# Kernel tuning notes

Measured on AMD Instinct MI355X. Metric: run time of the kernel, lower is better.

## Reference

```python
import jax, jax.numpy as jnp
import numpy as np

KH, KW = 3, 3
H_OUT, W_OUT = 62, 62

def setup_inputs() -> dict:
    key = jax.random.key(0)
    k1, k2 = jax.random.split(key)
    x = jax.random.normal(k1, (16, 32, 64, 64), dtype=jnp.float32)
    weight = jax.random.normal(k2, (H_OUT, W_OUT, 64, 32, KH, KW), dtype=jnp.float32) * 0.01
    return {"x": x, "weight": weight}

def reference(x, weight):
    # Unfold: patches[b,c,kh,kw,i,j] = x[b,c,i+kh,j+kw]; small fixed 3x3 loop is fine.
    patches = jnp.stack([
        jnp.stack([x[:, :, kh:kh + H_OUT, kw:kw + W_OUT] for kw in range(KW)], axis=2)
        for kh in range(KH)
    ], axis=2)  # [B, C_in, kH, kW, H_out, W_out]
    # Per-position (no weight sharing) contraction over c_in, kh, kw.
    out = jnp.einsum('bcklij,ijockl->boij', patches, weight)
    return jax.nn.sigmoid(out)
```

## Files before the change

### kernel.cpp

```cpp
#include <hip/hip_runtime.h>

#define HO 62
#define WO 62
#define CIN 32
#define COUT 64
#define BATCH 16
#define KROW 288
#define JT 4
#define COLS 6

typedef float f4a4 __attribute__((ext_vector_type(4), aligned(4)));

__global__ __launch_bounds__(256, 4)
void lc2d_kernel(const float* __restrict__ x,
                 const float* __restrict__ wgt,
                 float* __restrict__ out) {
    __shared__ __align__(16) float win[CIN][3][COLS][BATCH];

    const int blk = blockIdx.x;
    const int i  = blk % HO;
    const int j0 = (blk / HO) * JT;

    const int t = threadIdx.x;

    for (int r = t; r < BATCH * CIN * 3; r += 256) {
        const int b   = r & 15;
        const int ckh = r >> 4;
        const int c   = ckh / 3;
        const int kh  = ckh % 3;
        const float* src = x + (((b * CIN + c) * 64) + (i + kh)) * 64;
        #pragma unroll
        for (int cc = 0; cc < COLS; cc++) {
            int col = j0 + cc;
            if (col > 63) col = 63;
            win[c][kh][cc][b] = src[col];
        }
    }
    __syncthreads();

    const int wsel = t >> 6;
    const int o    = t & 63;

    const float* wj[JT];
    #pragma unroll
    for (int jj = 0; jj < JT; jj++) {
        int pj = i * WO + (j0 + jj);
        if (pj > HO * WO - 1) pj = HO * WO - 1;
        wj[jj] = wgt + (size_t)pj * (COUT * KROW) + o * KROW;
    }

    float acc[JT][4];
    #pragma unroll
    for (int jj = 0; jj < JT; jj++)
        #pragma unroll
        for (int bb = 0; bb < 4; bb++) acc[jj][bb] = 0.0f;

    const float* xbase = &win[0][0][0][wsel * 4];

    for (int c = 0; c < CIN; c++) {
        float wq[JT][9];
        #pragma unroll
        for (int jj = 0; jj < JT; jj++) {
            const float* p = wj[jj] + c * 9;
            const f4a4 wA = *(const f4a4*)p;
            const f4a4 wB = *(const f4a4*)(p + 4);
            wq[jj][0] = wA.x; wq[jj][1] = wA.y; wq[jj][2] = wA.z; wq[jj][3] = wA.w;
            wq[jj][4] = wB.x; wq[jj][5] = wB.y; wq[jj][6] = wB.z; wq[jj][7] = wB.w;
            wq[jj][8] = p[8];
        }
        #pragma unroll
        for (int kh = 0; kh < 3; kh++) {
            float4 xv[COLS];
            const float* xb = xbase + (c * 3 + kh) * (COLS * BATCH);
            #pragma unroll
            for (int cc = 0; cc < COLS; cc++)
                xv[cc] = *(const float4*)(xb + cc * BATCH);
            #pragma unroll
            for (int jj = 0; jj < JT; jj++) {
                #pragma unroll
                for (int kw = 0; kw < 3; kw++) {
                    const float w = wq[jj][kh * 3 + kw];
                    const float4 xx = xv[jj + kw];
                    acc[jj][0] += w * xx.x;
                    acc[jj][1] += w * xx.y;
                    acc[jj][2] += w * xx.z;
                    acc[jj][3] += w * xx.w;
                }
            }
        }
    }

    #pragma unroll
    for (int bb = 0; bb < 4; bb++) {
        const int b = wsel * 4 + bb;
        float* op = out + (((size_t)(b * COUT + o) * HO + i) * WO + j0);
        float2 s0;
        s0.x = 1.0f / (1.0f + __expf(-acc[0][bb]));
        s0.y = 1.0f / (1.0f + __expf(-acc[1][bb]));
        *(float2*)op = s0;
        if (j0 + 3 < WO) {
            float2 s1;
            s1.x = 1.0f / (1.0f + __expf(-acc[2][bb]));
            s1.y = 1.0f / (1.0f + __expf(-acc[3][bb]));
            *((float2*)op + 1) = s1;
        }
    }
}

extern "C" void kernel_launch(void* const* d_in, const int* in_sizes, int n_in,
                              void* d_out, int out_size, void* d_ws, size_t ws_size,
                              hipStream_t stream) {
    const float* x   = (const float*)d_in[0];
    const float* wgt = (const float*)d_in[1];
    float* out       = (float*)d_out;
    const int grid = HO * ((WO + JT - 1) / JT);
    lc2d_kernel<<<dim3(grid), dim3(256), 0, stream>>>(x, wgt, out);
}
```

Measured before the change: 571.7 us.

## Stream weights into LDS with async global_load_lds double buffering and XCD remap

Weights are now staged into a swizzled, double-buffered LDS tile with direct global-to-LDS loads, prefetching the next two-channel phase while the current one is computed. The x input window is no longer staged in shared memory and is read directly from global memory per batch. The tile width drops from four to two output columns, and block indices are remapped so neighbouring tiles share an XCD. The goal is coalesced, overlapped weight streaming from HBM, at the cost of more blocks, more per-phase barriers, and redundant x reads from global memory or cache.

```diff
diff --git a/kernel.cpp b/kernel.cpp
--- a/kernel.cpp
+++ b/kernel.cpp
@@ -1,4 +1,5 @@
 #include <hip/hip_runtime.h>
+#include <stdint.h>
 
 #define HO 62
 #define WO 62
@@ -6,48 +7,64 @@
 #define COUT 64
 #define BATCH 16
 #define KROW 288
-#define JT 4
-#define COLS 6
+#define JT 2
+#define NJT (WO / JT)
+#define ROWS 128
+#define PC 2
+#define NPH (CIN / PC)
+#define PH_DW (PC * 9)
+#define RSTRIDE 32
+#define SLOTS (ROWS * RSTRIDE)
+#define NXCD 8
 
-typedef float f4a4 __attribute__((ext_vector_type(4), aligned(4)));
+typedef const __attribute__((address_space(1))) void* gptr_t;
+typedef __attribute__((address_space(3))) void* lptr_t;
 
 __global__ __launch_bounds__(256, 4)
 void lc2d_kernel(const float* __restrict__ x,
                  const float* __restrict__ wgt,
                  float* __restrict__ out) {
-    __shared__ __align__(16) float win[CIN][3][COLS][BATCH];
+    __shared__ __align__(16) float wlds[2][SLOTS];
 
-    const int blk = blockIdx.x;
-    const int i  = blk % HO;
-    const int j0 = (blk / HO) * JT;
+    const int orig = blockIdx.x;
+    const int nwg  = HO * NJT;
+    const int qch  = nwg / NXCD, rch = nwg % NXCD;
+    const int xcd  = orig % NXCD, pos = orig / NXCD;
+    const int wg   = ((xcd < rch) ? xcd * (qch + 1)
+                                  : rch * (qch + 1) + (xcd - rch) * qch) + pos;
+    const int i  = wg / NJT;
+    const int j0 = (wg % NJT) * JT;
 
-    const int t = threadIdx.x;
-
-    for (int r = t; r < BATCH * CIN * 3; r += 256) {
-        const int b   = r & 15;
-        const int ckh = r >> 4;
-        const int c   = ckh / 3;
-        const int kh  = ckh % 3;
-        const float* src = x + (((b * CIN + c) * 64) + (i + kh)) * 64;
-        #pragma unroll
-        for (int cc = 0; cc < COLS; cc++) {
-            int col = j0 + cc;
-            if (col > 63) col = 63;
-            win[c][kh][cc][b] = src[col];
-        }
-    }
-    __syncthreads();
-
+    const int t    = threadIdx.x;
     const int wsel = t >> 6;
     const int o    = t & 63;
+    const int ws_u = __builtin_amdgcn_readfirstlane(wsel);
 
-    const float* wj[JT];
+    const float* wbase = wgt + (size_t)(i * WO + j0) * (COUT * KROW);
+
+    int goff[16];
     #pragma unroll
-    for (int jj = 0; jj < JT; jj++) {
-        int pj = i * WO + (j0 + jj);
-        if (pj > HO * WO - 1) pj = HO * WO - 1;
-        wj[jj] = wgt + (size_t)pj * (COUT * KROW) + o * KROW;
+    for (int g = 0; g < 16; g++) {
+        const int s   = wsel * 1024 + g * 64 + o;
+        const int row = s >> 5;
+        const int k   = s & 31;
+        const int l   = k ^ ((row & 7) << 2);
+        int src;
+        if (l < 24) {
+            const int cc = l / 12;
+            int r2 = l % 12; if (r2 > 8) r2 = 8;
+            src = row * KROW + cc * 9 + r2;
+        } else {
+            src = row * KROW;
+        }
+        goff[g] = src;
     }
+
+    #pragma unroll
+    for (int g = 0; g < 16; g++)
+        __builtin_amdgcn_global_load_lds((gptr_t)(wbase + goff[g]),
+                                         (lptr_t)&wlds[0][ws_u * 1024 + g * 64],
+                                         4, 0, 0);
 
     float acc[JT][4];
     #pragma unroll
@@ -55,55 +72,81 @@
         #pragma unroll
         for (int bb = 0; bb < 4; bb++) acc[jj][bb] = 0.0f;
 
-    const float* xbase = &win[0][0][0][wsel * 4];
+    const float* xp[4];
+    #pragma unroll
+    for (int bb = 0; bb < 4; bb++)
+        xp[bb] = x + ((size_t)(wsel * 4 + bb) * CIN) * 4096 + i * 64 + j0;
 
-    for (int c = 0; c < CIN; c++) {
-        float wq[JT][9];
+    const int swz = (o & 7) << 2;
+
+    __syncthreads();
+
+    int cur = 0;
+    for (int p = 0; p < NPH; p++) {
+        if (p + 1 < NPH) {
+            const float* wsrc = wbase + (p + 1) * PH_DW;
+            #pragma unroll
+            for (int g = 0; g < 16; g++)
+                __builtin_amdgcn_global_load_lds((gptr_t)(wsrc + goff[g]),
+                                                 (lptr_t)&wlds[cur ^ 1][ws_u * 1024 + g * 64],
+                                                 4, 0, 0);
+        }
+
         #pragma unroll
-        for (int jj = 0; jj < JT; jj++) {
-            const float* p = wj[jj] + c * 9;
-            const f4a4 wA = *(const f4a4*)p;
-            const f4a4 wB = *(const f4a4*)(p + 4);
-            wq[jj][0] = wA.x; wq[jj][1] = wA.y; wq[jj][2] = wA.z; wq[jj][3] = wA.w;
-            wq[jj][4] = wB.x; wq[jj][5] = wB.y; wq[jj][6] = wB.z; wq[jj][7] = wB.w;
-            wq[jj][8] = p[8];
-        }
-        #pragma unroll
-        for (int kh = 0; kh < 3; kh++) {
-            float4 xv[COLS];
-            const float* xb = xbase + (c * 3 + kh) * (COLS * BATCH);
-            #pragma unroll
-            for (int cc = 0; cc < COLS; cc++)
-                xv[cc] = *(const float4*)(xb + cc * BATCH);
+        for (int cc = 0; cc < PC; cc++) {
+            const int c = p * PC + cc;
+
+            float4 wA[JT], wB[JT]; float w8[JT];
             #pragma unroll
             for (int jj = 0; jj < JT; jj++) {
+                const int base = (jj * 64 + o) * RSTRIDE + cc * 12;
+                wA[jj] = *(const float4*)&wlds[cur][(base + 0) ^ swz];
+                wB[jj] = *(const float4*)&wlds[cur][(base + 4) ^ swz];
+                w8[jj] = wlds[cur][(base + 8) ^ swz];
+            }
+
+            #pragma unroll
+            for (int kh = 0; kh < 3; kh++) {
+                float2 xa[4], xb[4];
                 #pragma unroll
-                for (int kw = 0; kw < 3; kw++) {
-                    const float w = wq[jj][kh * 3 + kw];
-                    const float4 xx = xv[jj + kw];
-                    acc[jj][0] += w * xx.x;
-                    acc[jj][1] += w * xx.y;
-                    acc[jj][2] += w * xx.z;
-                    acc[jj][3] += w * xx.w;
+                for (int bb = 0; bb < 4; bb++) {
+                    const float* xr = xp[bb] + (c * 64 + kh) * 64;
+                    xa[bb] = *(const float2*)xr;
+                    xb[bb] = *(const float2*)(xr + 2);
+                }
+                #pragma unroll
+                for (int jj = 0; jj < JT; jj++) {
+                    #pragma unroll
+                    for (int kw = 0; kw < 3; kw++) {
+                        const int q = kh * 3 + kw;
+                        const float w = (q < 4) ? ((const float*)&wA[jj])[q]
+                                      : (q < 8) ? ((const float*)&wB[jj])[q - 4]
+                                                : w8[jj];
+                        const int col = jj + kw;
+                        #pragma unroll
+                        for (int bb = 0; bb < 4; bb++) {
+                            const float xv = (col == 0) ? xa[bb].x
+                                           : (col == 1) ? xa[bb].y
+                                           : (col == 2) ? xb[bb].x
+                                                        : xb[bb].y;
+                            acc[jj][bb] += w * xv;
+                        }
+                    }
                 }
             }
         }
+        __syncthreads();
+        cur ^= 1;
     }
 
     #pragma unroll
     for (int bb = 0; bb < 4; bb++) {
         const int b = wsel * 4 + bb;
         float* op = out + (((size_t)(b * COUT + o) * HO + i) * WO + j0);
-        float2 s0;
-        s0.x = 1.0f / (1.0f + __expf(-acc[0][bb]));
-        s0.y = 1.0f / (1.0f + __expf(-acc[1][bb]));
-        *(float2*)op = s0;
-        if (j0 + 3 < WO) {
-            float2 s1;
-            s1.x = 1.0f / (1.0f + __expf(-acc[2][bb]));
-            s1.y = 1.0f / (1.0f + __expf(-acc[3][bb]));
-            *((float2*)op + 1) = s1;
-        }
+        float2 s;
+        s.x = 1.0f / (1.0f + __expf(-acc[0][bb]));
+        s.y = 1.0f / (1.0f + __expf(-acc[1][bb]));
+        *(float2*)op = s;
     }
 }
 
@@ -113,6 +156,6 @@
     const float* x   = (const float*)d_in[0];
     const float* wgt = (const float*)d_in[1];
     float* out       = (float*)d_out;
-    const int grid = HO * ((WO + JT - 1) / JT);
+    const int grid = HO * NJT;
     lc2d_kernel<<<dim3(grid), dim3(256), 0, stream>>>(x, wgt, out);
 }
```

Measured after the change: 482.0 us. 15.7% less time.

## Restructure local conv into single-wave blocks over two columns with XCD-aware remap

Applied to the files above, without the earlier changes.

Replaces the 256-thread, shared-memory-staged kernel with 64-thread workgroups. Each thread handles one output channel across all 16 batch items for two adjacent output columns, reading x straight from global memory with no LDS and no barrier. Weights are loaded as aligned 16-byte vectors in chunks of 4 input channels, and block IDs are remapped so neighbouring tiles stay on the same XCD and share L2. The aim is to cut LDS and synchronisation overhead and improve weight streaming, at the cost of redundant global reads of x and higher register pressure.

```diff
diff --git a/kernel.cpp b/kernel.cpp
--- a/kernel.cpp
+++ b/kernel.cpp
@@ -6,104 +6,75 @@
 #define COUT 64
 #define BATCH 16
 #define KROW 288
-#define JT 4
-#define COLS 6
+#define NJT 31
+#define NXCD 8
 
-typedef float f4a4 __attribute__((ext_vector_type(4), aligned(4)));
+typedef float f4w __attribute__((ext_vector_type(4), aligned(16)));
+typedef float f4x __attribute__((ext_vector_type(4), aligned(8)));
 
-__global__ __launch_bounds__(256, 4)
+#define WSEL(arr, idx) (arr[(idx) >> 2][(idx) & 3])
+
+__global__ __launch_bounds__(64, 2)
 void lc2d_kernel(const float* __restrict__ x,
                  const float* __restrict__ wgt,
                  float* __restrict__ out) {
-    __shared__ __align__(16) float win[CIN][3][COLS][BATCH];
+    const int orig = blockIdx.x;
+    const int nwg  = HO * NJT;
+    const int qch  = nwg / NXCD, rch = nwg % NXCD;
+    const int xcd  = orig % NXCD, cpos = orig / NXCD;
+    const int wg   = ((xcd < rch) ? xcd * (qch + 1)
+                                  : rch * (qch + 1) + (xcd - rch) * qch) + cpos;
+    const int i  = wg / NJT;
+    const int j0 = (wg % NJT) * 2;
+    const int pj = i * WO + j0;
 
-    const int blk = blockIdx.x;
-    const int i  = blk % HO;
-    const int j0 = (blk / HO) * JT;
+    const int o = threadIdx.x;
 
-    const int t = threadIdx.x;
+    const float* w0 = wgt + ((size_t)pj * COUT + o) * KROW;
+    const float* w1 = w0 + (size_t)COUT * KROW;
 
-    for (int r = t; r < BATCH * CIN * 3; r += 256) {
-        const int b   = r & 15;
-        const int ckh = r >> 4;
-        const int c   = ckh / 3;
-        const int kh  = ckh % 3;
-        const float* src = x + (((b * CIN + c) * 64) + (i + kh)) * 64;
+    const float* xb[BATCH];
+    #pragma unroll
+    for (int b = 0; b < BATCH; ++b) xb[b] = x + (size_t)b * (CIN * 64 * 64);
+
+    float a0[BATCH], a1[BATCH];
+    #pragma unroll
+    for (int b = 0; b < BATCH; ++b) { a0[b] = 0.0f; a1[b] = 0.0f; }
+
+    for (int ch = 0; ch < 8; ++ch) {
+        f4w wa[9], wb[9];
         #pragma unroll
-        for (int cc = 0; cc < COLS; cc++) {
-            int col = j0 + cc;
-            if (col > 63) col = 63;
-            win[c][kh][cc][b] = src[col];
-        }
-    }
-    __syncthreads();
-
-    const int wsel = t >> 6;
-    const int o    = t & 63;
-
-    const float* wj[JT];
-    #pragma unroll
-    for (int jj = 0; jj < JT; jj++) {
-        int pj = i * WO + (j0 + jj);
-        if (pj > HO * WO - 1) pj = HO * WO - 1;
-        wj[jj] = wgt + (size_t)pj * (COUT * KROW) + o * KROW;
-    }
-
-    float acc[JT][4];
-    #pragma unroll
-    for (int jj = 0; jj < JT; jj++)
-        #pragma unroll
-        for (int bb = 0; bb < 4; bb++) acc[jj][bb] = 0.0f;
-
-    const float* xbase = &win[0][0][0][wsel * 4];
-
-    for (int c = 0; c < CIN; c++) {
-        float wq[JT][9];
-        #pragma unroll
-        for (int jj = 0; jj < JT; jj++) {
-            const float* p = wj[jj] + c * 9;
-            const f4a4 wA = *(const f4a4*)p;
-            const f4a4 wB = *(const f4a4*)(p + 4);
-            wq[jj][0] = wA.x; wq[jj][1] = wA.y; wq[jj][2] = wA.z; wq[jj][3] = wA.w;
-            wq[jj][4] = wB.x; wq[jj][5] = wB.y; wq[jj][6] = wB.z; wq[jj][7] = wB.w;
-            wq[jj][8] = p[8];
+        for (int q = 0; q < 9; ++q) {
+            wa[q] = *(const f4w*)(w0 + ch * 36 + q * 4);
+            wb[q] = *(const f4w*)(w1 + ch * 36 + q * 4);
         }
         #pragma unroll
-        for (int kh = 0; kh < 3; kh++) {
-            float4 xv[COLS];
-            const float* xb = xbase + (c * 3 + kh) * (COLS * BATCH);
+        for (int cc = 0; cc < 4; ++cc) {
             #pragma unroll
-            for (int cc = 0; cc < COLS; cc++)
-                xv[cc] = *(const float4*)(xb + cc * BATCH);
-            #pragma unroll
-            for (int jj = 0; jj < JT; jj++) {
+            for (int kh = 0; kh < 3; ++kh) {
+                const int off = (((ch * 4 + cc) * 64) + i + kh) * 64 + j0;
+                const int kb  = cc * 9 + kh * 3;
                 #pragma unroll
-                for (int kw = 0; kw < 3; kw++) {
-                    const float w = wq[jj][kh * 3 + kw];
-                    const float4 xx = xv[jj + kw];
-                    acc[jj][0] += w * xx.x;
-                    acc[jj][1] += w * xx.y;
-                    acc[jj][2] += w * xx.z;
-                    acc[jj][3] += w * xx.w;
+                for (int b = 0; b < BATCH; ++b) {
+                    const f4x xv = *(const f4x*)(xb[b] + off);
+                    a0[b] += WSEL(wa, kb + 0) * xv.x;
+                    a0[b] += WSEL(wa, kb + 1) * xv.y;
+                    a0[b] += WSEL(wa, kb + 2) * xv.z;
+                    a1[b] += WSEL(wb, kb + 0) * xv.y;
+                    a1[b] += WSEL(wb, kb + 1) * xv.z;
+                    a1[b] += WSEL(wb, kb + 2) * xv.w;
                 }
             }
         }
     }
 
     #pragma unroll
-    for (int bb = 0; bb < 4; bb++) {
-        const int b = wsel * 4 + bb;
-        float* op = out + (((size_t)(b * COUT + o) * HO + i) * WO + j0);
-        float2 s0;
-        s0.x = 1.0f / (1.0f + __expf(-acc[0][bb]));
-        s0.y = 1.0f / (1.0f + __expf(-acc[1][bb]));
-        *(float2*)op = s0;
-        if (j0 + 3 < WO) {
-            float2 s1;
-            s1.x = 1.0f / (1.0f + __expf(-acc[2][bb]));
-            s1.y = 1.0f / (1.0f + __expf(-acc[3][bb]));
-            *((float2*)op + 1) = s1;
-        }
+    for (int b = 0; b < BATCH; ++b) {
+        float* op = out + (size_t)(b * COUT + o) * (HO * WO) + pj;
+        float2 s;
+        s.x = 1.0f / (1.0f + __expf(-a0[b]));
+        s.y = 1.0f / (1.0f + __expf(-a1[b]));
+        *(float2*)op = s;
     }
 }
 
@@ -113,6 +84,6 @@
     const float* x   = (const float*)d_in[0];
     const float* wgt = (const float*)d_in[1];
     float* out       = (float*)d_out;
-    const int grid = HO * ((WO + JT - 1) / JT);
-    lc2d_kernel<<<dim3(grid), dim3(256), 0, stream>>>(x, wgt, out);
+    const int grid = HO * NJT;
+    lc2d_kernel<<<dim3(grid), dim3(64), 0, stream>>>(x, wgt, out);
 }
```

Result: faster. 556.3 us (-2.7%).
